# Kernel optimization log

Measured on AMD Instinct MI355X. Metric: run time of the kernel, lower is better.

Reference implementation:

```python
import jax, jax.numpy as jnp
import numpy as np
from jax import lax


def _conv(x, w, b, pad=1):
    y = lax.conv_general_dilated(x, w, (1, 1), [(pad, pad), (pad, pad)],
                                 dimension_numbers=('NCHW', 'OIHW', 'NCHW'))
    return y + b[None, :, None, None]


def _lrelu(x):
    return jnp.where(x >= 0, x, 0.2 * x)


def _up2(x):
    # bilinear x2 upsample, align_corners=False (PyTorch F.interpolate semantics)
    def along(v, axis):
        n = v.shape[axis]
        c = jnp.clip((jnp.arange(2 * n, dtype=jnp.float32) + 0.5) / 2.0 - 0.5, 0.0, n - 1.0)
        i0 = jnp.floor(c).astype(jnp.int32)
        i1 = jnp.minimum(i0 + 1, n - 1)
        t = c - i0.astype(jnp.float32)
        sh = [1] * v.ndim
        sh[axis] = 2 * n
        t = t.reshape(sh)
        return jnp.take(v, i0, axis=axis) * (1.0 - t) + jnp.take(v, i1, axis=axis) * t
    return along(along(x, 2), 3)


def _deform_conv(x, off_feat, ow, ob, w, b, groups=8):
    # Modulated deformable conv v2 (DCNv2), k=3, stride=1, pad=1, dil=1.
    B, C, H, W = x.shape
    G, K = groups, 9
    cg = C // G
    om = _conv(off_feat, ow, ob, pad=1)              # [B, 3*G*K, H, W]
    o1, o2, m = jnp.split(om, 3, axis=1)
    mask = jax.nn.sigmoid(m).reshape(B, G, 1, K, H, W)
    dy = o1.reshape(B, G, K, H, W)
    dx = o2.reshape(B, G, K, H, W)
    k = jnp.arange(K)
    ky = (k // 3 - 1).astype(jnp.float32)[:, None, None]   # [K,1,1]
    kx = (k % 3 - 1).astype(jnp.float32)[:, None, None]
    hh = jnp.arange(H, dtype=jnp.float32)[None, :, None]
    ww = jnp.arange(W, dtype=jnp.float32)[None, None, :]
    py = dy + (hh + ky)[None, None]                  # [B,G,K,H,W]
    px = dx + (ww + kx)[None, None]
    y0 = jnp.floor(py)
    x0 = jnp.floor(px)
    ty = py - y0
    tx = px - x0
    y0i = y0.astype(jnp.int32)
    x0i = x0.astype(jnp.int32)
    xf = x.reshape(B, G, cg, H * W)
    def gather(yi, xi):
        valid = (yi >= 0) & (yi < H) & (xi >= 0) & (xi < W)
        idx = jnp.clip(yi, 0, H - 1) * W + jnp.clip(xi, 0, W - 1)
        idx = idx.reshape(B, G, 1, K * H * W)
        v = jnp.take_along_axis(xf, idx, axis=3).reshape(B, G, cg, K, H, W)
        return v * valid[:, :, None].astype(x.dtype)
    w00 = ((1 - ty) * (1 - tx))[:, :, None]
    w01 = ((1 - ty) * tx)[:, :, None]
    w10 = (ty * (1 - tx))[:, :, None]
    w11 = (ty * tx)[:, :, None]
    val = (gather(y0i, x0i) * w00 + gather(y0i, x0i + 1) * w01 +
           gather(y0i + 1, x0i) * w10 + gather(y0i + 1, x0i + 1) * w11)
    val = val * mask                                  # [B,G,cg,K,H,W]
    O = w.shape[0]
    wr = w.reshape(O, G, cg, K)
    return jnp.einsum('ogck,bgckhw->bohw', wr, val) + b[None, :, None, None]


def setup_inputs() -> dict:
    key = jax.random.key(0)
    ks = jax.random.split(key, 18)
    B, C, H, W = 2, 32, 256, 256
    G, K = 8, 9
    def Wi(k, shape, scale=1.0):
        fan = int(np.prod(shape[1:]))
        return jax.random.normal(k, shape, jnp.float32) * np.float32(scale / np.sqrt(fan))
    def Bi(k, n):
        return jax.random.normal(k, (n,), jnp.float32) * 0.01
    return {
        'short_fea': jax.random.normal(ks[0], (B, C, H, W), jnp.float32),
        'long_fea': jax.random.normal(ks[1], (B, C, H, W), jnp.float32),
        'prev_offset': jax.random.normal(ks[2], (B, 32, H // 2, W // 2), jnp.float32),
        'conv1_w': Wi(ks[3], (C, 2 * C, 1, 1)),
        'conv1_b': Bi(ks[4], C),
        'oc1_w': Wi(ks[5], (32, C, 3, 3)),
        'oc1_b': Bi(ks[6], 32),
        'oc2_w': Wi(ks[7], (32, 64, 3, 3)),
        'oc2_b': Bi(ks[8], 32),
        'oc3_w': Wi(ks[9], (32, 32, 3, 3)),
        'oc3_b': Bi(ks[10], 32),
        'dcn_off_w': Wi(ks[11], (3 * G * K, 32, 3, 3), scale=0.1),
        'dcn_off_b': Bi(ks[12], 3 * G * K),
        'dcn_w': Wi(ks[13], (C, C, 3, 3)),
        'dcn_b': Bi(ks[14], C),
    }


def reference(short_fea, long_fea, prev_offset, conv1_w, conv1_b, oc1_w, oc1_b,
              oc2_w, oc2_b, oc3_w, oc3_b, dcn_off_w, dcn_off_b, dcn_w, dcn_b):
    comb = jnp.concatenate([short_fea, long_fea], axis=1)
    off = _conv(comb, conv1_w, conv1_b, pad=0)                 # 1x1
    off = _lrelu(_conv(off, oc1_w, oc1_b, pad=1))
    prev = _up2(prev_offset)
    off = _lrelu(_conv(jnp.concatenate([off, prev * 2.0], axis=1), oc2_w, oc2_b, pad=1))
    off = _lrelu(_conv(off, oc3_w, oc3_b, pad=1))
    out = _lrelu(_deform_conv(long_fea, off, dcn_off_w, dcn_off_b, dcn_w, dcn_b, groups=8))
    return (out, off)
```

## Files before the change

### kernel.cpp

```cpp
#include <hip/hip_runtime.h>

#define HH 256
#define WW 256
#define HWSZ (HH*WW)
#define CH 32

typedef __attribute__((ext_vector_type(8))) short bfrag;
typedef __attribute__((ext_vector_type(4))) float f32x4;

__device__ __forceinline__ float lrelu_f(float x){ return x >= 0.f ? x : 0.2f*x; }

__device__ __forceinline__ unsigned short bf16_rne(float f){
    unsigned int u = __float_as_uint(f);
    unsigned int r = (u + 0x7fffu + ((u >> 16) & 1u)) >> 16;
    return (unsigned short)r;
}
__device__ __forceinline__ float bf16_to_f(unsigned short h){
    return __uint_as_float(((unsigned int)h) << 16);
}


__global__ __launch_bounds__(256) void conv1x1_kernel(
    const float* __restrict__ s, const float* __restrict__ l,
    const float* __restrict__ w, const float* __restrict__ bias,
    float* __restrict__ y)
{
    int gid = blockIdx.x*256 + threadIdx.x;
    int b = gid >> 16;
    int pix = gid & (HWSZ-1);
    const float* sp = s + (size_t)b*CH*HWSZ + pix;
    const float* lp = l + (size_t)b*CH*HWSZ + pix;
    float acc[CH];
    #pragma unroll
    for (int o=0;o<CH;++o) acc[o] = bias[o];
    for (int c=0;c<CH;++c) {
        float v = sp[(size_t)c*HWSZ];
        #pragma unroll
        for (int o=0;o<CH;++o) acc[o] += w[o*64+c]*v;
    }
    for (int c=0;c<CH;++c) {
        float v = lp[(size_t)c*HWSZ];
        #pragma unroll
        for (int o=0;o<CH;++o) acc[o] += w[o*64+32+c]*v;
    }
    float* yp = y + (size_t)b*CH*HWSZ + pix;
    #pragma unroll
    for (int o=0;o<CH;++o) yp[(size_t)o*HWSZ] = acc[o];
}

template<int NP>
__global__ __launch_bounds__(256) void conv3x3_kernel(
    const float* __restrict__ x0, const float* __restrict__ x1,
    const float* __restrict__ w, const float* __restrict__ bias,
    float* __restrict__ y, int relu)
{
    int gid = blockIdx.x*256 + threadIdx.x;
    int b = gid >> 16;
    int pix = gid & (HWSZ-1);
    int h = pix >> 8, cw = pix & 255;
    const int CIN = 32*NP;
    float acc[CH];
    #pragma unroll
    for (int o=0;o<CH;++o) acc[o] = bias[o];
    #pragma unroll
    for (int p=0;p<NP;++p) {
        const float* src = (p==0) ? x0 : x1;
        const float* xb = src + (size_t)b*CH*HWSZ;
        for (int c=0;c<CH;++c) {
            const float* xp = xb + (size_t)c*HWSZ;
            float v[9];
            #pragma unroll
            for (int t=0;t<9;++t) {
                int hh = h + t/3 - 1;
                int wx = cw + t%3 - 1;
                v[t] = (hh>=0 && hh<HH && wx>=0 && wx<WW) ? xp[hh*WW+wx] : 0.f;
            }
            const float* wp = w + (size_t)(p*32 + c)*9;
            #pragma unroll
            for (int o=0;o<CH;++o) {
                #pragma unroll
                for (int t=0;t<9;++t)
                    acc[o] += wp[(size_t)o*CIN*9 + t] * v[t];
            }
        }
    }
    float* yp = y + (size_t)b*CH*HWSZ + pix;
    #pragma unroll
    for (int o=0;o<CH;++o)
        yp[(size_t)o*HWSZ] = relu ? lrelu_f(acc[o]) : acc[o];
}

__global__ __launch_bounds__(256) void up2_kernel(
    const float* __restrict__ x, float* __restrict__ y)
{
    int gid = blockIdx.x*256 + threadIdx.x;
    int ow = gid & 255;
    int oh = (gid >> 8) & 255;
    int bc = gid >> 16;
    const int Hin = 128, Win = 128;
    float cy = (oh + 0.5f)*0.5f - 0.5f;
    float cx = (ow + 0.5f)*0.5f - 0.5f;
    cy = fminf(fmaxf(cy, 0.f), (float)(Hin-1));
    cx = fminf(fmaxf(cx, 0.f), (float)(Win-1));
    int y0 = (int)floorf(cy);
    int x0 = (int)floorf(cx);
    int y1 = min(y0+1, Hin-1);
    int x1 = min(x0+1, Win-1);
    float ty = cy - (float)y0, tx = cx - (float)x0;
    const float* xp = x + (size_t)bc*Hin*Win;
    float v00 = xp[y0*Win+x0], v01 = xp[y0*Win+x1];
    float v10 = xp[y1*Win+x0], v11 = xp[y1*Win+x1];
    float v = v00*(1.f-ty)*(1.f-tx) + v01*(1.f-ty)*tx + v10*ty*(1.f-tx) + v11*ty*tx;
    y[gid] = 2.0f*v;
}

__global__ __launch_bounds__(256) void dcn_off_kernel(
    const float* __restrict__ x, const float* __restrict__ w,
    const float* __restrict__ bias, float* __restrict__ om,
    int r0, int rows)
{
    int b = blockIdx.x / rows;
    int rr = blockIdx.x % rows;
    int cw = threadIdx.x;
    int h = r0 + rr;
    int oc0 = blockIdx.y*24;
    const float* xb = x + (size_t)b*CH*HWSZ;
    float* omb = om + (size_t)b*216*rows*WW;
    float acc[24];
    #pragma unroll
    for (int j=0;j<24;++j) acc[j] = bias[oc0+j];
    for (int c=0;c<32;++c) {
        const float* xp = xb + (size_t)c*HWSZ;
        float v[9];
        #pragma unroll
        for (int t=0;t<9;++t) {
            int hh = h + t/3 - 1;
            int wx = cw + t%3 - 1;
            v[t] = (hh>=0 && hh<HH && wx>=0 && wx<WW) ? xp[hh*WW+wx] : 0.f;
        }
        const float* wpp = w + (size_t)c*9;
        #pragma unroll
        for (int j=0;j<24;++j) {
            #pragma unroll
            for (int t=0;t<9;++t)
                acc[j] += wpp[(size_t)(oc0+j)*288 + t] * v[t];
        }
    }
    #pragma unroll
    for (int j=0;j<24;++j)
        omb[(size_t)(oc0+j)*rows*WW + (size_t)rr*WW + cw] = acc[j];
}

__global__ __launch_bounds__(256) void dcn_kernel(
    const float* __restrict__ x, const float* __restrict__ om,
    const float* __restrict__ w, const float* __restrict__ bias,
    float* __restrict__ y, int r0, int rows)
{
    const int b  = blockIdx.z;
    const int os = blockIdx.y;
    const int rowsWW = rows*WW;
    int rr = blockIdx.x;
    int cw = threadIdx.x;
    int h = r0 + rr;
    const float* xb  = x  + (size_t)b*CH*HWSZ;
    const float* omb = om + (size_t)b*216*rowsWW;
    int ppos = rr*WW + cw;
    int ob = os*16;

    float acc[16];
    #pragma unroll
    for (int o=0;o<16;++o) acc[o] = bias[ob+o];

    for (int g=0; g<8; ++g) {
        const float* xg = xb + (size_t)g*4*HWSZ;
        #pragma unroll
        for (int k=0;k<9;++k) {
            int oc = g*9+k;
            float dy = omb[(size_t)oc*rowsWW + ppos];
            float dx = omb[(size_t)(72+oc)*rowsWW + ppos];
            float mm = omb[(size_t)(144+oc)*rowsWW + ppos];
            mm = 1.f/(1.f + __expf(-mm));
            float py = dy + (float)(h + k/3 - 1);
            float px = dx + (float)(cw + k%3 - 1);
            float y0f = floorf(py), x0f = floorf(px);
            int yi = (int)y0f, xi = (int)x0f;
            float ty = py - y0f, tx = px - x0f;
            float w00 = (1.f-ty)*(1.f-tx), w01 = (1.f-ty)*tx;
            float w10 = ty*(1.f-tx),       w11 = ty*tx;
            int yc0 = min(max(yi,0),HH-1),   yc1 = min(max(yi+1,0),HH-1);
            int xc0 = min(max(xi,0),WW-1),   xc1 = min(max(xi+1,0),WW-1);
            bool vy0 = (yi>=0)&&(yi<HH),     vy1 = (yi+1>=0)&&(yi+1<HH);
            bool vx0 = (xi>=0)&&(xi<WW),     vx1 = (xi+1>=0)&&(xi+1<WW);
            float f00 = (vy0&&vx0)? w00*mm : 0.f;
            float f01 = (vy0&&vx1)? w01*mm : 0.f;
            float f10 = (vy1&&vx0)? w10*mm : 0.f;
            float f11 = (vy1&&vx1)? w11*mm : 0.f;
            int i00 = yc0*WW+xc0, i01 = yc0*WW+xc1;
            int i10 = yc1*WW+xc0, i11 = yc1*WW+xc1;
            #pragma unroll
            for (int c=0;c<4;++c) {
                const float* xc = xg + (size_t)c*HWSZ;
                float val = xc[i00]*f00 + xc[i01]*f01 + xc[i10]*f10 + xc[i11]*f11;
                const float* wpp = w + (size_t)(g*4+c)*9 + k;
                #pragma unroll
                for (int o=0;o<16;++o)
                    acc[o] += wpp[(size_t)(ob+o)*288] * val;
            }
        }
    }

    float* yb = y + (size_t)(b*CH + ob)*HWSZ + (size_t)h*WW;
    #pragma unroll
    for (int o=0;o<16;++o)
        yb[(size_t)o*HWSZ + cw] = lrelu_f(acc[o]);
}


__global__ __launch_bounds__(256) void pack_w_bf16(
    const float* __restrict__ dow, unsigned short* __restrict__ wp)
{
    int gid = blockIdx.x*256 + threadIdx.x;
    if (gid >= 9*14*64) return;
    int l = gid & 63;
    int rest = gid >> 6;
    int nt = rest % 14;
    int ks = rest / 14;
    int oc = nt*16 + (l & 15);
    int c0 = 8*(l >> 4);
    unsigned short outv[8];
    #pragma unroll
    for (int j=0;j<8;++j) {
        float v = (oc < 216) ? dow[(size_t)oc*288 + (size_t)(c0+j)*9 + ks] : 0.f;
        outv[j] = bf16_rne(v);
    }
    unsigned short* dst = wp + (size_t)gid*8;
    #pragma unroll
    for (int j=0;j<8;++j) dst[j] = outv[j];
}

__global__ __launch_bounds__(256) void pack_conv_hl(
    const float* __restrict__ w, unsigned short* __restrict__ wphi,
    unsigned short* __restrict__ wplo, int TAPS, int F)
{
    int total = TAPS*F*2*64;
    int gid = blockIdx.x*256 + threadIdx.x;
    if (gid >= total) return;
    int l = gid & 63;
    int q = gid >> 6;
    int nt = q & 1;
    int p = q >> 1;
    int f = p % F;
    int ks = p / F;
    int oc = nt*16 + (l & 15);
    int CIN = F*32;
    unsigned short hv[8], lv[8];
    #pragma unroll
    for (int j=0;j<8;++j) {
        int c = f*32 + (l>>4)*8 + j;
        float v = w[(size_t)oc*CIN*TAPS + (size_t)c*TAPS + ks];
        unsigned short h = bf16_rne(v);
        hv[j] = h;
        lv[j] = bf16_rne(v - bf16_to_f(h));
    }
    unsigned short* dh = wphi + (size_t)gid*8;
    unsigned short* dl = wplo + (size_t)gid*8;
    #pragma unroll
    for (int j=0;j<8;++j) { dh[j] = hv[j]; dl[j] = lv[j]; }
}

__global__ __launch_bounds__(256) void pack_wg(
    const float* __restrict__ dcw, unsigned short* __restrict__ wgh,
    unsigned short* __restrict__ wgl)
{
    int gid = blockIdx.x*256 + threadIdx.x;
    if (gid >= 1152) return;
    int l = gid & 63;
    int q = gid >> 6;
    int nt = q & 1;
    int ks = q >> 1;
    int oc = nt*16 + (l & 15);
    unsigned short hv[8], lv[8];
    #pragma unroll
    for (int j=0;j<8;++j) {
        int K = ks*32 + (l>>4)*8 + j;
        int g = K/36;
        int rem = K - g*36;
        int kk = rem >> 2;
        int c = rem & 3;
        float v = dcw[(size_t)oc*288 + (size_t)(g*4+c)*9 + kk];
        unsigned short h = bf16_rne(v);
        hv[j] = h;
        lv[j] = bf16_rne(v - bf16_to_f(h));
    }
    unsigned short* dh = wgh + (size_t)gid*8;
    unsigned short* dl = wgl + (size_t)gid*8;
    #pragma unroll
    for (int j=0;j<8;++j) { dh[j] = hv[j]; dl[j] = lv[j]; }
}

__global__ __launch_bounds__(256) void conv1_fused(
    const float* __restrict__ s, const float* __restrict__ l,
    const float* __restrict__ w, const float* __restrict__ bias,
    unsigned short* __restrict__ t0)
{
    int gid = blockIdx.x*256 + threadIdx.x;
    int b = gid >> 16;
    int pix = gid & (HWSZ-1);
    const float* sp = s + (size_t)b*CH*HWSZ + pix;
    const float* lp = l + (size_t)b*CH*HWSZ + pix;
    float acc[CH];
    #pragma unroll
    for (int o=0;o<CH;++o) acc[o] = bias[o];
    for (int c=0;c<CH;++c) {
        float v = sp[(size_t)c*HWSZ];
        #pragma unroll
        for (int o=0;o<CH;++o) acc[o] += w[o*64+c]*v;
    }
    for (int c=0;c<CH;++c) {
        float v = lp[(size_t)c*HWSZ];
        #pragma unroll
        for (int o=0;o<CH;++o) acc[o] += w[o*64+32+c]*v;
    }
    unsigned short* op = t0 + (size_t)gid*64;
    #pragma unroll
    for (int cb=0; cb<4; ++cb) {
        unsigned short hv[8], lv[8];
        #pragma unroll
        for (int j=0;j<8;++j) {
            float v = acc[cb*8+j];
            unsigned short h = bf16_rne(v);
            hv[j] = h;
            lv[j] = bf16_rne(v - bf16_to_f(h));
        }
        *reinterpret_cast<uint4*>(op + cb*8)      = *reinterpret_cast<uint4*>(hv);
        *reinterpret_cast<uint4*>(op + 32 + cb*8) = *reinterpret_cast<uint4*>(lv);
    }
}

__global__ __launch_bounds__(256) void up2_hl(
    const float* __restrict__ x, unsigned short* __restrict__ xq)
{
    int gid = blockIdx.x*256 + threadIdx.x;
    int b = gid >> 16;
    int pix = gid & (HWSZ-1);
    int oh = pix >> 8, ow = pix & 255;
    const int Hin = 128, Win = 128;
    float cy = (oh + 0.5f)*0.5f - 0.5f;
    float cx = (ow + 0.5f)*0.5f - 0.5f;
    cy = fminf(fmaxf(cy, 0.f), (float)(Hin-1));
    cx = fminf(fmaxf(cx, 0.f), (float)(Win-1));
    int y0 = (int)floorf(cy);
    int x0 = (int)floorf(cx);
    int y1 = min(y0+1, Hin-1);
    int x1 = min(x0+1, Win-1);
    float ty = cy - (float)y0, tx = cx - (float)x0;
    float w00 = (1.f-ty)*(1.f-tx), w01 = (1.f-ty)*tx;
    float w10 = ty*(1.f-tx),       w11 = ty*tx;
    unsigned short* op = xq + (size_t)gid*128;
    const float* xb = x + (size_t)b*32*Hin*Win;
    #pragma unroll
    for (int cb=0; cb<4; ++cb) {
        unsigned short hv[8], lv[8];
        #pragma unroll
        for (int j=0;j<8;++j) {
            const float* xp = xb + (size_t)(cb*8+j)*Hin*Win;
            float v = 2.0f*(xp[y0*Win+x0]*w00 + xp[y0*Win+x1]*w01 +
                            xp[y1*Win+x0]*w10 + xp[y1*Win+x1]*w11);
            unsigned short h = bf16_rne(v);
            hv[j] = h;
            lv[j] = bf16_rne(v - bf16_to_f(h));
        }
        *reinterpret_cast<uint4*>(op + 32 + cb*8)      = *reinterpret_cast<uint4*>(hv);
        *reinterpret_cast<uint4*>(op + 96 + cb*8)      = *reinterpret_cast<uint4*>(lv);
    }
}

template<int TAPS, int F, bool RELU, bool NCHW_OUT, bool LO_OUT>
__global__ __launch_bounds__(256) void conv_mfma(
    const unsigned short* __restrict__ xq,
    const unsigned short* __restrict__ wphi,
    const unsigned short* __restrict__ wplo,
    const float* __restrict__ bias,
    unsigned short* __restrict__ yq, int ochs, int ohioff, int oloff,
    float* __restrict__ ynchw)
{
    int bid = blockIdx.x;
    int wq = bid & 3;
    int h  = (bid >> 2) & 255;
    int b  = bid >> 10;
    int wv = threadIdx.x >> 6;
    int l  = threadIdx.x & 63;
    int w0 = wq*64 + wv*16;
    int lw = l & 15;
    int lq = l >> 4;
    const int CHS = 2*F*32;

    f32x4 acc[2];
    acc[0] = (f32x4){0.f,0.f,0.f,0.f};
    acc[1] = (f32x4){0.f,0.f,0.f,0.f};

    const unsigned short* xb = xq + (size_t)b*HWSZ*CHS;
    const bfrag zero = {0,0,0,0,0,0,0,0};

    #pragma unroll 3
    for (int ks=0; ks<TAPS; ++ks) {
        int dy = (TAPS==9) ? ks/3 - 1 : 0;
        int dx = (TAPS==9) ? ks%3 - 1 : 0;
        int hh = h + dy;
        if (hh < 0 || hh >= HH) continue;
        int wx = w0 + lw + dx;
        bool vw = (wx >= 0) && (wx < WW);
        int wxc = min(max(wx, 0), WW-1);
        const unsigned short* xp = xb + ((size_t)hh*WW + wxc)*CHS + lq*8;
        bfrag bh[F], bl[F];
        #pragma unroll
        for (int f=0;f<F;++f) {
            bh[f] = *reinterpret_cast<const bfrag*>(xp + f*32);
            bl[f] = *reinterpret_cast<const bfrag*>(xp + F*32 + f*32);
            bh[f] = vw ? bh[f] : zero;
            bl[f] = vw ? bl[f] : zero;
        }
        #pragma unroll
        for (int nt=0; nt<2; ++nt) {
            #pragma unroll
            for (int f=0;f<F;++f) {
                size_t widx = ((size_t)((ks*F + f)*2 + nt)*64 + l)*8;
                bfrag ah = *reinterpret_cast<const bfrag*>(wphi + widx);
                bfrag al = *reinterpret_cast<const bfrag*>(wplo + widx);
                acc[nt] = __builtin_amdgcn_mfma_f32_16x16x32_bf16(ah, bh[f], acc[nt], 0, 0, 0);
                acc[nt] = __builtin_amdgcn_mfma_f32_16x16x32_bf16(ah, bl[f], acc[nt], 0, 0, 0);
                acc[nt] = __builtin_amdgcn_mfma_f32_16x16x32_bf16(al, bh[f], acc[nt], 0, 0, 0);
            }
        }
    }

    int pw = w0 + lw;
    size_t pix = (size_t)h*WW + pw;
    #pragma unroll
    for (int nt=0; nt<2; ++nt) {
        float yv[4];
        #pragma unroll
        for (int i=0;i<4;++i) {
            int oc = nt*16 + lq*4 + i;
            float v = acc[nt][i] + bias[oc];
            yv[i] = RELU ? lrelu_f(v) : v;
        }
        unsigned short hv[4], lv[4];
        #pragma unroll
        for (int i=0;i<4;++i) {
            unsigned short hbits = bf16_rne(yv[i]);
            hv[i] = hbits;
            lv[i] = bf16_rne(yv[i] - bf16_to_f(hbits));
        }
        size_t obase = ((size_t)b*HWSZ + pix)*ochs + nt*16 + lq*4;
        *reinterpret_cast<ushort4*>(yq + obase + ohioff) = *reinterpret_cast<ushort4*>(hv);
        if (LO_OUT)
            *reinterpret_cast<ushort4*>(yq + obase + oloff) = *reinterpret_cast<ushort4*>(lv);
        if (NCHW_OUT) {
            #pragma unroll
            for (int i=0;i<4;++i) {
                int oc = nt*16 + lq*4 + i;
                ynchw[((size_t)(b*32 + oc))*HWSZ + pix] = yv[i];
            }
        }
    }
}

__global__ __launch_bounds__(256) void dcn_off_mfma(
    const unsigned short* __restrict__ xq,
    const unsigned short* __restrict__ wp,
    const float* __restrict__ bias,
    unsigned short* __restrict__ om,
    int r0, int rows)
{
    int bid = blockIdx.x;
    int wq = bid & 3;
    int rloc = (bid >> 2) % rows;
    int b  = (bid >> 2) / rows;
    int h  = r0 + rloc;
    int wv = threadIdx.x >> 6;
    int l  = threadIdx.x & 63;
    int w0 = wq*64 + wv*16;
    int lw = l & 15;
    int lq = l >> 4;

    f32x4 acc[14];
    #pragma unroll
    for (int t=0;t<14;++t) acc[t] = (f32x4){0.f,0.f,0.f,0.f};

    const unsigned short* xb = xq + (size_t)b*HWSZ*32;
    const bfrag zero = {0,0,0,0,0,0,0,0};

    #pragma unroll 1
    for (int ks=0; ks<9; ++ks) {
        int dy = ks/3 - 1, dx = ks%3 - 1;
        int hh = h + dy;
        if (hh < 0 || hh >= HH) continue;
        int wx = w0 + lw + dx;
        bool vw = (wx >= 0) && (wx < WW);
        int wxc = min(max(wx, 0), WW-1);
        const unsigned short* xp = xb + ((size_t)hh*WW + wxc)*32 + lq*8;
        bfrag bfr = *reinterpret_cast<const bfrag*>(xp);
        bfr = vw ? bfr : zero;
        const unsigned short* wks = wp + (size_t)ks*14*64*8;
        #pragma unroll
        for (int nt=0; nt<14; ++nt) {
            bfrag afr = *reinterpret_cast<const bfrag*>(wks + ((size_t)nt*64 + l)*8);
            acc[nt] = __builtin_amdgcn_mfma_f32_16x16x32_bf16(afr, bfr, acc[nt], 0, 0, 0);
        }
    }

    unsigned short* omb = om + (size_t)b*216*HWSZ;
    size_t pbase = (size_t)h*WW + w0 + lw;
    #pragma unroll
    for (int nt=0; nt<14; ++nt) {
        #pragma unroll
        for (int i=0;i<4;++i) {
            int oc = nt*16 + lq*4 + i;
            if (oc < 216)
                omb[(size_t)oc*HWSZ + pbase] = bf16_rne(acc[nt][i] + bias[oc]);
        }
    }
}

__global__ __launch_bounds__(256) void dcn_sample(
    const float* __restrict__ x,
    const unsigned short* __restrict__ om,
    unsigned int* __restrict__ vhi,
    unsigned int* __restrict__ vlo,
    int r0, int rows)
{
    const int b = blockIdx.z;
    const int k = blockIdx.y;
    int rr = blockIdx.x;
    int cw = threadIdx.x;
    int h = r0 + rr;
    const float* xb = x + (size_t)b*CH*HWSZ;
    const unsigned short* omb = om + (size_t)b*216*HWSZ;
    int ppos = h*WW + cw;
    size_t rowsWW = (size_t)rows*WW;
    size_t lpix = (size_t)rr*WW + cw;
    unsigned int* vhb = vhi + (size_t)b*144*rowsWW;
    unsigned int* vlb = vlo + (size_t)b*144*rowsWW;

    for (int g=0; g<8; ++g) {
        const float* xg = xb + (size_t)g*4*HWSZ;
        int oc = g*9+k;
        float dy = bf16_to_f(omb[(size_t)oc*HWSZ + ppos]);
        float dx = bf16_to_f(omb[(size_t)(72+oc)*HWSZ + ppos]);
        float mm = bf16_to_f(omb[(size_t)(144+oc)*HWSZ + ppos]);
        mm = 1.f/(1.f + __expf(-mm));
        float py = dy + (float)(h + k/3 - 1);
        float px = dx + (float)(cw + k%3 - 1);
        float y0f = floorf(py), x0f = floorf(px);
        int yi = (int)y0f, xi = (int)x0f;
        float ty = py - y0f, tx = px - x0f;
        float w00 = (1.f-ty)*(1.f-tx), w01 = (1.f-ty)*tx;
        float w10 = ty*(1.f-tx),       w11 = ty*tx;
        int yc0 = min(max(yi,0),HH-1),   yc1 = min(max(yi+1,0),HH-1);
        int xc0 = min(max(xi,0),WW-1),   xc1 = min(max(xi+1,0),WW-1);
        bool vy0 = (yi>=0)&&(yi<HH),     vy1 = (yi+1>=0)&&(yi+1<HH);
        bool vx0 = (xi>=0)&&(xi<WW),     vx1 = (xi+1>=0)&&(xi+1<WW);
        float f00 = (vy0&&vx0)? w00*mm : 0.f;
        float f01 = (vy0&&vx1)? w01*mm : 0.f;
        float f10 = (vy1&&vx0)? w10*mm : 0.f;
        float f11 = (vy1&&vx1)? w11*mm : 0.f;
        int i00 = yc0*WW+xc0, i01 = yc0*WW+xc1;
        int i10 = yc1*WW+xc0, i11 = yc1*WW+xc1;
        float val[4];
        #pragma unroll
        for (int c=0;c<4;++c) {
            const float* xc = xg + (size_t)c*HWSZ;
            val[c] = xc[i00]*f00 + xc[i01]*f01 + xc[i10]*f10 + xc[i11]*f11;
        }
        unsigned short h0 = bf16_rne(val[0]);
        unsigned short h1 = bf16_rne(val[1]);
        unsigned short h2 = bf16_rne(val[2]);
        unsigned short h3 = bf16_rne(val[3]);
        unsigned short l0 = bf16_rne(val[0] - bf16_to_f(h0));
        unsigned short l1 = bf16_rne(val[1] - bf16_to_f(h1));
        unsigned short l2 = bf16_rne(val[2] - bf16_to_f(h2));
        unsigned short l3 = bf16_rne(val[3] - bf16_to_f(h3));
        size_t r0w = (size_t)(oc*2)*rowsWW + lpix;
        size_t r1w = (size_t)(oc*2+1)*rowsWW + lpix;
        vhb[r0w] = (unsigned)h0 | ((unsigned)h1 << 16);
        vhb[r1w] = (unsigned)h2 | ((unsigned)h3 << 16);
        vlb[r0w] = (unsigned)l0 | ((unsigned)l1 << 16);
        vlb[r1w] = (unsigned)l2 | ((unsigned)l3 << 16);
    }
}

__global__ __launch_bounds__(256) void dcn_gemm(
    const unsigned int* __restrict__ vhi,
    const unsigned int* __restrict__ vlo,
    const unsigned short* __restrict__ wgh,
    const unsigned short* __restrict__ wgl,
    const float* __restrict__ bias,
    float* __restrict__ y,
    int r0, int rows)
{
    int bid = blockIdx.x;
    int wq = bid & 3;
    int rloc = (bid >> 2) % rows;
    int b  = (bid >> 2) / rows;
    int h  = r0 + rloc;
    int wv = threadIdx.x >> 6;
    int l  = threadIdx.x & 63;
    int w0 = wq*64 + wv*16;
    int lw = l & 15;
    int lq = l >> 4;
    size_t rowsWW = (size_t)rows*WW;
    const unsigned int* vhb = vhi + (size_t)b*144*rowsWW;
    const unsigned int* vlb = vlo + (size_t)b*144*rowsWW;
    size_t p = (size_t)rloc*WW + w0 + lw;

    f32x4 acc[2];
    acc[0] = (f32x4){0.f,0.f,0.f,0.f};
    acc[1] = (f32x4){0.f,0.f,0.f,0.f};

    #pragma unroll 3
    for (int ks=0; ks<9; ++ks) {
        int urow = ks*16 + lq*4;
        __attribute__((aligned(16))) unsigned int uh[4], ul[4];
        #pragma unroll
        for (int j=0;j<4;++j) {
            uh[j] = vhb[(size_t)(urow+j)*rowsWW + p];
            ul[j] = vlb[(size_t)(urow+j)*rowsWW + p];
        }
        bfrag bh = *reinterpret_cast<const bfrag*>(uh);
        bfrag bl = *reinterpret_cast<const bfrag*>(ul);
        const unsigned short* wk_h = wgh + (size_t)ks*2*64*8;
        const unsigned short* wk_l = wgl + (size_t)ks*2*64*8;
        #pragma unroll
        for (int nt=0; nt<2; ++nt) {
            bfrag ah = *reinterpret_cast<const bfrag*>(wk_h + ((size_t)nt*64 + l)*8);
            bfrag al = *reinterpret_cast<const bfrag*>(wk_l + ((size_t)nt*64 + l)*8);
            acc[nt] = __builtin_amdgcn_mfma_f32_16x16x32_bf16(ah, bh, acc[nt], 0, 0, 0);
            acc[nt] = __builtin_amdgcn_mfma_f32_16x16x32_bf16(ah, bl, acc[nt], 0, 0, 0);
            acc[nt] = __builtin_amdgcn_mfma_f32_16x16x32_bf16(al, bh, acc[nt], 0, 0, 0);
        }
    }

    float* yb = y + (size_t)b*CH*HWSZ + (size_t)h*WW + w0 + lw;
    #pragma unroll
    for (int nt=0; nt<2; ++nt) {
        #pragma unroll
        for (int i=0;i<4;++i) {
            int oc = nt*16 + lq*4 + i;
            yb[(size_t)oc*HWSZ] = lrelu_f(acc[nt][i] + bias[oc]);
        }
    }
}

extern "C" void kernel_launch(void* const* d_in, const int* in_sizes, int n_in,
                              void* d_out, int out_size, void* d_ws, size_t ws_size,
                              hipStream_t stream)
{
    (void)in_sizes; (void)n_in; (void)out_size;
    const float* short_fea = (const float*)d_in[0];
    const float* long_fea  = (const float*)d_in[1];
    const float* prev      = (const float*)d_in[2];
    const float* conv1_w   = (const float*)d_in[3];
    const float* conv1_b   = (const float*)d_in[4];
    const float* oc1_w     = (const float*)d_in[5];
    const float* oc1_b     = (const float*)d_in[6];
    const float* oc2_w     = (const float*)d_in[7];
    const float* oc2_b     = (const float*)d_in[8];
    const float* oc3_w     = (const float*)d_in[9];
    const float* oc3_b     = (const float*)d_in[10];
    const float* dow       = (const float*)d_in[11];
    const float* dob       = (const float*)d_in[12];
    const float* dcw       = (const float*)d_in[13];
    const float* dcb       = (const float*)d_in[14];

    float* out = (float*)d_out;
    float* off_out = out + (size_t)2*CH*HWSZ;

    const int CROWS = 128;
    size_t om_b   = (size_t)2*216*HWSZ*2;
    size_t cat_b  = (size_t)2*HWSZ*128*2;
    size_t t_b    = (size_t)2*HWSZ*64*2;
    size_t xo_b   = (size_t)2*HWSZ*32*2;
    size_t val_b  = (size_t)2*144*CROWS*WW*4;
    size_t wpk_b  = (size_t)9*14*64*8*2;
    size_t wo1_b  = (size_t)9*1*2*64*8*2;
    size_t wo2_b  = (size_t)9*2*2*64*8*2;
    size_t wo3_b  = (size_t)9*1*2*64*8*2;
    size_t wg_b   = (size_t)9*2*64*8*2;
    size_t needed = om_b + xo_b + 2*val_b + wpk_b + 2*(wo1_b+wo2_b+wo3_b) + 2*wg_b;

    if (ws_size >= needed && om_b >= cat_b + t_b) {
        char* p = (char*)d_ws;
        unsigned short* om = (unsigned short*)p;
        unsigned short* cat  = (unsigned short*)p;
        unsigned short* tbuf = (unsigned short*)(p + cat_b);
        p += om_b;
        unsigned short* xqo = (unsigned short*)p;  p += xo_b;
        unsigned int* vhi = (unsigned int*)p;      p += val_b;
        unsigned int* vlo = (unsigned int*)p;      p += val_b;
        unsigned short* wpk = (unsigned short*)p;  p += wpk_b;
        unsigned short* wo1h = (unsigned short*)p; p += wo1_b;
        unsigned short* wo1l = (unsigned short*)p; p += wo1_b;
        unsigned short* wo2h = (unsigned short*)p; p += wo2_b;
        unsigned short* wo2l = (unsigned short*)p; p += wo2_b;
        unsigned short* wo3h = (unsigned short*)p; p += wo3_b;
        unsigned short* wo3l = (unsigned short*)p; p += wo3_b;
        unsigned short* wgh = (unsigned short*)p;  p += wg_b;
        unsigned short* wgl = (unsigned short*)p;

        pack_conv_hl<<<5, 256, 0, stream>>>(oc1_w, wo1h, wo1l, 9, 1);
        pack_conv_hl<<<9, 256, 0, stream>>>(oc2_w, wo2h, wo2l, 9, 2);
        pack_conv_hl<<<5, 256, 0, stream>>>(oc3_w, wo3h, wo3l, 9, 1);
        pack_w_bf16<<<32, 256, 0, stream>>>(dow, wpk);
        pack_wg<<<5, 256, 0, stream>>>(dcw, wgh, wgl);

        const int PIX_BLOCKS = (2*HWSZ)/256;
        const int CONV_BLOCKS = 2*HH*4;

        conv1_fused<<<PIX_BLOCKS, 256, 0, stream>>>(short_fea, long_fea, conv1_w, conv1_b, tbuf);
        conv_mfma<9,1,true,false,true><<<CONV_BLOCKS, 256, 0, stream>>>(
            tbuf, wo1h, wo1l, oc1_b, cat, 128, 0, 64, nullptr);
        up2_hl<<<PIX_BLOCKS, 256, 0, stream>>>(prev, cat);
        conv_mfma<9,2,true,false,true><<<CONV_BLOCKS, 256, 0, stream>>>(
            cat, wo2h, wo2l, oc2_b, tbuf, 64, 0, 32, nullptr);
        conv_mfma<9,1,true,true,false><<<CONV_BLOCKS, 256, 0, stream>>>(
            tbuf, wo3h, wo3l, oc3_b, xqo, 32, 0, 0, off_out);

        dcn_off_mfma<<<2*HH*4, 256, 0, stream>>>(xqo, wpk, dob, om, 0, HH);

        for (int r0 = 0; r0 < HH; r0 += CROWS) {
            dim3 gs(CROWS, 9, 2);
            dcn_sample<<<gs, 256, 0, stream>>>(long_fea, om, vhi, vlo, r0, CROWS);
            dcn_gemm<<<2*CROWS*4, 256, 0, stream>>>(vhi, vlo, wgh, wgl, dcb, out, r0, CROWS);
        }
    } else {
        float* bufB = (float*)d_ws;
        float* bufU = bufB + (size_t)2*CH*HWSZ;
        float* om   = bufU + (size_t)2*CH*HWSZ;
        size_t used = (size_t)2 * 2*CH*HWSZ * sizeof(float);
        size_t avail = (ws_size > used) ? (ws_size - used) : 0;
        const int PIX_BLOCKS = (2*HWSZ)/256;

        conv1x1_kernel<<<PIX_BLOCKS, 256, 0, stream>>>(short_fea, long_fea, conv1_w, conv1_b, out);
        conv3x3_kernel<1><<<PIX_BLOCKS, 256, 0, stream>>>(out, nullptr, oc1_w, oc1_b, bufB, 1);
        up2_kernel<<<(2*CH*HWSZ)/256, 256, 0, stream>>>(prev, bufU);
        conv3x3_kernel<2><<<PIX_BLOCKS, 256, 0, stream>>>(bufB, bufU, oc2_w, oc2_b, out, 1);
        conv3x3_kernel<1><<<PIX_BLOCKS, 256, 0, stream>>>(out, nullptr, oc3_w, oc3_b, off_out, 1);

        size_t per_row = (size_t)216 * WW * sizeof(float);
        int rows_chunk = (int)(avail / per_row);
        if (rows_chunk < 1) rows_chunk = 1;
        if (rows_chunk > HH) rows_chunk = HH;
        for (int b=0;b<2;++b) {
            const float* offb = off_out + (size_t)b*CH*HWSZ;
            const float* lfb  = long_fea + (size_t)b*CH*HWSZ;
            float* outb = out + (size_t)b*CH*HWSZ;
            for (int r0=0;r0<HH;r0+=rows_chunk) {
                int rows = (HH - r0 < rows_chunk) ? (HH - r0) : rows_chunk;
                dim3 g1(rows, 9);
                dcn_off_kernel<<<g1, 256, 0, stream>>>(offb, dow, dob, om, r0, rows);
                dim3 g2f(rows, 2, 1);
                dcn_kernel<<<g2f, 256, 0, stream>>>(lfb, om, dcw, dcb, outb, r0, rows);
            }
        }
    }
}
```

Before: 345.8 us.

## Stage 3-row input halo tile in LDS for MFMA convolution

The conv_mfma kernel now cooperatively loads a 3x66-pixel halo tile of the bf16 hi/lo input into shared memory, zero-filling out-of-bounds positions, before the tap loop. Each tap then reads its B fragments from LDS instead of global memory, which removes per-tap bounds checks and repeated global reads of overlapping neighbours. Records are padded by 8 shorts to reduce bank conflicts. In exchange it adds a sync, a sizeable LDS allocation (about 51 KB for F=2) that may limit occupancy, and for the 1x1 case it loads two unused rows.

```diff
diff --git a/kernel.cpp b/kernel.cpp
--- a/kernel.cpp
+++ b/kernel.cpp
@@ -384,41 +384,55 @@
     unsigned short* __restrict__ yq, int ochs, int ohioff, int oloff,
     float* __restrict__ ynchw)
 {
+    constexpr int CHS = 2*F*32;
+    constexpr int REC = CHS + 8;
+    __shared__ unsigned short lds[3*66*REC];
+
     int bid = blockIdx.x;
     int wq = bid & 3;
     int h  = (bid >> 2) & 255;
     int b  = bid >> 10;
     int wv = threadIdx.x >> 6;
     int l  = threadIdx.x & 63;
-    int w0 = wq*64 + wv*16;
+    int blk_w0 = wq*64;
     int lw = l & 15;
     int lq = l >> 4;
-    const int CHS = 2*F*32;
+
+    const unsigned short* xb = xq + (size_t)b*HWSZ*CHS;
+
+    constexpr int CH8 = CHS/8;
+    constexpr int TOT = 3*66*CH8;
+    for (int idx = threadIdx.x; idx < TOT; idx += 256) {
+        int rec = idx / CH8;
+        int off = (idx - rec*CH8)*8;
+        int row = rec / 66;
+        int j   = rec - row*66;
+        int hh = h - 1 + row;
+        int wx = blk_w0 - 1 + j;
+        uint4 v = {0u,0u,0u,0u};
+        if (hh >= 0 && hh < HH && wx >= 0 && wx < WW)
+            v = *reinterpret_cast<const uint4*>(xb + ((size_t)hh*WW + wx)*CHS + off);
+        *reinterpret_cast<uint4*>(&lds[(size_t)rec*REC + off]) = v;
+    }
+    __syncthreads();
 
     f32x4 acc[2];
     acc[0] = (f32x4){0.f,0.f,0.f,0.f};
     acc[1] = (f32x4){0.f,0.f,0.f,0.f};
 
-    const unsigned short* xb = xq + (size_t)b*HWSZ*CHS;
-    const bfrag zero = {0,0,0,0,0,0,0,0};
+    int jbase = wv*16 + lw;
 
     #pragma unroll 3
     for (int ks=0; ks<TAPS; ++ks) {
-        int dy = (TAPS==9) ? ks/3 - 1 : 0;
-        int dx = (TAPS==9) ? ks%3 - 1 : 0;
-        int hh = h + dy;
-        if (hh < 0 || hh >= HH) continue;
-        int wx = w0 + lw + dx;
-        bool vw = (wx >= 0) && (wx < WW);
-        int wxc = min(max(wx, 0), WW-1);
-        const unsigned short* xp = xb + ((size_t)hh*WW + wxc)*CHS + lq*8;
+        int row  = (TAPS==9) ? ks/3 : 1;
+        int dxp1 = (TAPS==9) ? ks%3 : 1;
+        int rec = row*66 + jbase + dxp1;
+        const unsigned short* xp = &lds[(size_t)rec*REC + lq*8];
         bfrag bh[F], bl[F];
         #pragma unroll
         for (int f=0;f<F;++f) {
             bh[f] = *reinterpret_cast<const bfrag*>(xp + f*32);
             bl[f] = *reinterpret_cast<const bfrag*>(xp + F*32 + f*32);
-            bh[f] = vw ? bh[f] : zero;
-            bl[f] = vw ? bl[f] : zero;
         }
         #pragma unroll
         for (int nt=0; nt<2; ++nt) {
@@ -434,7 +448,7 @@
         }
     }
 
-    int pw = w0 + lw;
+    int pw = blk_w0 + jbase;
     size_t pix = (size_t)h*WW + pw;
     #pragma unroll
     for (int nt=0; nt<2; ++nt) {
```

New measurement: 321.7 us (median of 2 runs). 7.0% less time.
